# Kernel optimization log

Hardware: AMD Instinct MI355X
Metric: run time of the kernel (lower is better)

## Reference

```python
import jax, jax.numpy as jnp
import numpy as np

B, BAG, H, C = 512, 32, 1024, 53
EPS = 1e-8  # torch F.cosine_similarity denominator clamp


def setup_inputs() -> dict:
    key = jax.random.key(0)
    ks = jax.random.split(key, 5)
    return {
        "sent_reps": jax.random.normal(ks[0], (B, BAG, H), jnp.float32),
        "aug_sent_reps": jax.random.normal(ks[1], (B, BAG, H), jnp.float32),
        "rel_table": jax.random.normal(ks[2], (C, H), jnp.float32),
        "cls_w": jax.random.normal(ks[3], (C, H), jnp.float32) * 0.02,
        "cls_b": jnp.zeros((C,), jnp.float32),
        "labels": jax.random.randint(ks[4], (B,), 0, C),
        "temperature": jnp.asarray(0.1, jnp.float32),
    }


def _cl(rep, aug, bag_rep, T):
    # rep, aug: (B, bag, H); bag_rep: (B, H)
    nr = jnp.linalg.norm(rep, axis=-1)        # (B, bag)
    na = jnp.linalg.norm(aug, axis=-1)        # (B, bag)
    nb = jnp.linalg.norm(bag_rep, axis=-1)    # (B,)
    pos_sim = jnp.sum(rep * aug, axis=-1) / jnp.maximum(nr * na, EPS)  # (B, bag)
    pos = jnp.exp(pos_sim / T)
    # pair[c, j, b] = cos(rep[b, j], bag_rep[c])  -- matches torch permute/broadcast chain
    dots = jnp.einsum('bjh,ch->cjb', rep, bag_rep)               # (B, bag, B)
    denom = jnp.maximum(nb[:, None, None] * nr.T[None], EPS)      # (B, bag, B)
    pair = dots / denom
    idx = jnp.arange(rep.shape[0])
    axis_sim = pair[idx, :, idx]                                  # (B, bag): cos(rep[b,j], bag_rep[b])
    neg = jnp.exp(pair / T).sum(axis=2) - jnp.exp(axis_sim / T)   # (B, bag)
    return jnp.mean(-jnp.log(pos / (pos + neg)))


def reference(sent_reps, aug_sent_reps, rel_table, cls_w, cls_b, labels, temperature):
    # Selective attention per bag (scope slices are uniform bags of size BAG -> vectorized)
    rel = rel_table[labels]                                        # (B, H)
    scale = jnp.sqrt(jnp.asarray(H, sent_reps.dtype))
    scores = jnp.einsum('bh,bjh->bj', rel, sent_reps) / scale      # (B, bag)
    alphas = jax.nn.softmax(scores, axis=-1)
    bag_reps = jnp.einsum('bj,bjh->bh', alphas, sent_reps)         # (B, H)
    bag_out = bag_reps @ cls_w.T + cls_b                           # (B, C)  (dropout in eval = identity)
    cl_loss = _cl(sent_reps, aug_sent_reps, bag_reps, temperature)
    return bag_out, cl_loss
```

## Files before the change

### kernel.cpp

```cpp
#include <hip/hip_runtime.h>
#include <hip/hip_bf16.h>


typedef __bf16 bf16x8 __attribute__((ext_vector_type(8)));
typedef __bf16 bf16x4 __attribute__((ext_vector_type(4)));
typedef float  f32x4  __attribute__((ext_vector_type(4)));

__device__ inline float wsum(float v) {
    #pragma unroll
    for (int off = 32; off > 0; off >>= 1) v += __shfl_xor(v, off, 64);
    return v;
}

__device__ inline void gll16(const void* g, void* l) {
    __builtin_amdgcn_global_load_lds((const __attribute__((address_space(1))) void*)g,
                                     (__attribute__((address_space(3))) void*)l, 16, 0, 0);
}

__global__ __launch_bounds__(256) void k0_cvt(const float* __restrict__ w, __bf16* __restrict__ wb,
                                              float* __restrict__ nbsq)
{
    int i = blockIdx.x * 256 + threadIdx.x;
    wb[i] = (i < 53 * 1024) ? (__bf16)w[i] : (__bf16)0.0f;
    if (i < 512) nbsq[i] = 0.0f;
}

__global__ __launch_bounds__(256) void k12(
    const float* __restrict__ sent, const float* __restrict__ aug,
    const float* __restrict__ rel_table, const int* __restrict__ labels,
    __bf16* __restrict__ bagb, float* __restrict__ nbsq,
    __bf16* __restrict__ repb, float* __restrict__ nr, float* __restrict__ pos_sim,
    float* __restrict__ scoreg, float* __restrict__ alphag)
{
    __shared__ __bf16 Vb[32 * 1024];
    const int b = blockIdx.x, t = threadIdx.x;
    const int j = t >> 3, seg = t & 7;
    const int lane = t & 63;

    const size_t rbase = (size_t)(b * 32 + j) * 1024;
    const float* srow = sent + rbase;
    const float* arow = aug + rbase;
    const float* relp = rel_table + (size_t)labels[b] * 1024;

    float P = 0.f, R = 0.f, A = 0.f, D = 0.f;
    #pragma unroll 8
    for (int i = 0; i < 32; i++) {
        const int h = i * 32 + seg * 4;
        f32x4 v  = *(const f32x4*)(srow + h);
        f32x4 a  = *(const f32x4*)(arow + h);
        f32x4 rl = *(const f32x4*)(relp + h);
        P += v.x * rl.x + v.y * rl.y + v.z * rl.z + v.w * rl.w;
        R += v.x * v.x + v.y * v.y + v.z * v.z + v.w * v.w;
        A += a.x * a.x + a.y * a.y + a.z * a.z + a.w * a.w;
        D += v.x * a.x + v.y * a.y + v.z * a.z + v.w * a.w;
        bf16x4 vb = { (__bf16)v.x, (__bf16)v.y, (__bf16)v.z, (__bf16)v.w };
        *(bf16x4*)(&Vb[j * 1024 + (i ^ (j & 1)) * 32 + seg * 4]) = vb;
        *(bf16x4*)(repb + rbase + h) = vb;
    }
    #pragma unroll
    for (int off = 1; off <= 4; off <<= 1) {
        P += __shfl_xor(P, off, 64);
        R += __shfl_xor(R, off, 64);
        A += __shfl_xor(A, off, 64);
        D += __shfl_xor(D, off, 64);
    }
    if (seg == 0) {
        scoreg[b * 32 + j] = P * (1.0f / 32.0f);
        float nrv = sqrtf(R), nav = sqrtf(A);
        nr[b * 32 + j] = nrv;
        pos_sim[b * 32 + j] = D / fmaxf(nrv * nav, 1e-8f);
    }
    __threadfence_block();
    __syncthreads();

    if (t < 32) {
        float sj = scoreg[b * 32 + t];
        float m = sj;
        #pragma unroll
        for (int off = 16; off > 0; off >>= 1) m = fmaxf(m, __shfl_xor(m, off, 32));
        float e = __expf(sj - m);
        float sum = e;
        #pragma unroll
        for (int off = 16; off > 0; off >>= 1) sum += __shfl_xor(sum, off, 32);
        alphag[b * 32 + t] = e / sum;
    }
    __threadfence_block();
    __syncthreads();

    f32x4 bag = {0.f, 0.f, 0.f, 0.f};
    #pragma unroll 8
    for (int jj = 0; jj < 32; jj++) {
        const float al = alphag[b * 32 + jj];
        bf16x4 vb = *(const bf16x4*)(&Vb[jj * 1024 + ((t >> 3) ^ (jj & 1)) * 32 + (t & 7) * 4]);
        bag.x += al * (float)vb.x;
        bag.y += al * (float)vb.y;
        bag.z += al * (float)vb.z;
        bag.w += al * (float)vb.w;
    }
    bf16x4 bb = { (__bf16)bag.x, (__bf16)bag.y, (__bf16)bag.z, (__bf16)bag.w };
    *(bf16x4*)(bagb + (size_t)b * 1024 + t * 4) = bb;

    float q = bag.x * bag.x + bag.y * bag.y + bag.z * bag.z + bag.w * bag.w;
    q = wsum(q);
    if (lane == 0) atomicAdd(&nbsq[b], q);
}

__global__ __launch_bounds__(256) void k3m(
    const __bf16* __restrict__ bagb, const __bf16* __restrict__ cwb,
    const float* __restrict__ bias, float* __restrict__ out)
{
    __shared__ __align__(16) __bf16 Al[64 * 32];
    __shared__ __align__(16) __bf16 Bl[64 * 32];
    const int r0 = blockIdx.x * 64;
    const int t = threadIdx.x, lane = t & 63, w = t >> 6;
    const int m = lane & 15, quad = lane >> 4;
    f32x4 acc[4] = {};

    const int i0 = t * 8;
    const int row0 = i0 >> 5, kk0 = i0 & 31;
    const __bf16* gA = bagb + (size_t)(r0 + row0) * 1024 + kk0;
    const __bf16* gB = cwb + (size_t)row0 * 1024 + kk0;

    for (int k0 = 0; k0 < 1024; k0 += 32) {
        __syncthreads();
        gll16(gA + k0, Al + i0);
        gll16(gB + k0, Bl + i0);
        __syncthreads();
        bf16x8 a = *(const bf16x8*)(&Al[(w * 16 + m) * 32 + quad * 8]);
        #pragma unroll
        for (int n = 0; n < 4; n++) {
            bf16x8 bf = *(const bf16x8*)(&Bl[(n * 16 + m) * 32 + quad * 8]);
            acc[n] = __builtin_amdgcn_mfma_f32_16x16x32_bf16(a, bf, acc[n], 0, 0, 0);
        }
    }
    #pragma unroll
    for (int n = 0; n < 4; n++) {
        const int c = n * 16 + m;
        if (c < 53) {
            #pragma unroll
            for (int i = 0; i < 4; i++) {
                const int r = r0 + w * 16 + quad * 4 + i;
                out[(size_t)r * 53 + c] = acc[n][i] + bias[c];
            }
        }
    }
}

__global__ __launch_bounds__(256) void k4_gemm(
    const __bf16* __restrict__ repb, const __bf16* __restrict__ bagb,
    const float* __restrict__ nr, const float* __restrict__ nbsq,
    const float* __restrict__ temp, __bf16* __restrict__ E)
{
    __shared__ __align__(16) __bf16 Al[128 * 32];
    __shared__ __align__(16) __bf16 Bl[128 * 32];
    const int bid = blockIdx.x;
    const int xcd = bid & 7, slot = bid >> 3;
    const int cb = slot & 3, rb = (slot >> 2) * 8 + xcd;
    const int r0 = rb * 128, c0 = cb * 128;
    const int t = threadIdx.x, lane = t & 63, w = t >> 6;
    const int m = lane & 15, quad = lane >> 4;
    const int wr0 = (w & 1) * 64, wc0 = (w >> 1) * 64;

    f32x4 acc[4][4] = {};

    const int i0 = t * 8, i1 = 2048 + t * 8;
    const int row0 = i0 >> 5, kk0 = i0 & 31;
    const int row1 = i1 >> 5, kk1 = i1 & 31;
    const __bf16* gA0 = repb + (size_t)(r0 + row0) * 1024 + kk0;
    const __bf16* gA1 = repb + (size_t)(r0 + row1) * 1024 + kk1;
    const __bf16* gB0 = bagb + (size_t)(c0 + row0) * 1024 + kk0;
    const __bf16* gB1 = bagb + (size_t)(c0 + row1) * 1024 + kk1;

    for (int k0 = 0; k0 < 1024; k0 += 32) {
        __syncthreads();
        gll16(gA0 + k0, Al + i0);
        gll16(gA1 + k0, Al + i1);
        gll16(gB0 + k0, Bl + i0);
        gll16(gB1 + k0, Bl + i1);
        __syncthreads();
        bf16x8 a[4], bf[4];
        #pragma unroll
        for (int i = 0; i < 4; i++) a[i]  = *(const bf16x8*)(&Al[(wr0 + i * 16 + m) * 32 + quad * 8]);
        #pragma unroll
        for (int n = 0; n < 4; n++) bf[n] = *(const bf16x8*)(&Bl[(wc0 + n * 16 + m) * 32 + quad * 8]);
        #pragma unroll
        for (int i = 0; i < 4; i++)
            #pragma unroll
            for (int n = 0; n < 4; n++)
                acc[i][n] = __builtin_amdgcn_mfma_f32_16x16x32_bf16(a[i], bf[n], acc[i][n], 0, 0, 0);
    }

    const float invT = 1.0f / *temp;
    float nrv[16];
    #pragma unroll
    for (int i = 0; i < 4; i++)
        #pragma unroll
        for (int g = 0; g < 4; g++)
            nrv[i * 4 + g] = nr[r0 + wr0 + i * 16 + quad * 4 + g];
    #pragma unroll
    for (int n = 0; n < 4; n++) {
        const int c = c0 + wc0 + n * 16 + m;
        const float nbv = sqrtf(nbsq[c]);
        #pragma unroll
        for (int i = 0; i < 4; i++) {
            #pragma unroll
            for (int g = 0; g < 4; g++) {
                const int r = r0 + wr0 + i * 16 + quad * 4 + g;
                float pair = acc[i][n][g] / fmaxf(nbv * nrv[i * 4 + g], 1e-8f);
                E[(size_t)r * 512 + c] = (__bf16)__expf(pair * invT);
            }
        }
    }
}

__global__ __launch_bounds__(256) void k5_neg(
    const __bf16* __restrict__ E, const float* __restrict__ pos_sim,
    const float* __restrict__ temp, float* __restrict__ bsums)
{
    const int ct = blockIdx.x & 7, j = blockIdx.x >> 3;
    const int t = threadIdx.x, lane = t & 63, w = t >> 6;
    const int c8 = t & 7;
    const int bsub = t >> 3;
    const size_t cbase = (size_t)ct * 64 + c8 * 8;

    float acc[8] = {};
    #pragma unroll 4
    for (int it = 0; it < 16; it++) {
        const int b = it * 32 + bsub;
        bf16x8 v = *(const bf16x8*)(E + (size_t)(b * 32 + j) * 512 + cbase);
        #pragma unroll
        for (int k = 0; k < 8; k++) acc[k] += (float)v[k];
    }
    #pragma unroll
    for (int k = 0; k < 8; k++) {
        acc[k] += __shfl_xor(acc[k], 8, 64);
        acc[k] += __shfl_xor(acc[k], 16, 64);
        acc[k] += __shfl_xor(acc[k], 32, 64);
    }
    __shared__ float red[4][64];
    if (lane < 8) {
        #pragma unroll
        for (int k = 0; k < 8; k++) red[w][lane * 8 + k] = acc[k];
    }
    __syncthreads();

    if (t < 64) {
        const int cc = ct * 64 + t;
        float S = red[0][t] + red[1][t] + red[2][t] + red[3][t];
        S -= (float)E[(size_t)((cc << 5) + j) * 512 + cc];
        const float invT = 1.0f / *temp;
        const float lp = pos_sim[(cc << 5) + j] * invT;
        float term = logf(__expf(lp) + S) - lp;
        term = wsum(term);
        if (t == 0) bsums[blockIdx.x] = term;
    }
}

__global__ __launch_bounds__(256) void k6_final(const float* __restrict__ bsums, float* __restrict__ loss)
{
    const int t = threadIdx.x;
    float v = bsums[t];
    v = wsum(v);
    __shared__ float r[4];
    if ((t & 63) == 0) r[t >> 6] = v;
    __syncthreads();
    if (t == 0) *loss = (r[0] + r[1] + r[2] + r[3]) * (1.0f / 16384.0f);
}

extern "C" void kernel_launch(void* const* d_in, const int* in_sizes, int n_in,
                              void* d_out, int out_size, void* d_ws, size_t ws_size,
                              hipStream_t stream)
{
    const float* sent = (const float*)d_in[0];
    const float* aug  = (const float*)d_in[1];
    const float* rel  = (const float*)d_in[2];
    const float* clsw = (const float*)d_in[3];
    const float* clsb = (const float*)d_in[4];
    const int*   lab  = (const int*)d_in[5];
    const float* temp = (const float*)d_in[6];
    float* out = (float*)d_out;

    char* ws = (char*)d_ws;
    __bf16* bagb   = (__bf16*)(ws);
    float*  nbsq   = (float*)(ws + (1u << 20));
    float*  nr     = (float*)(ws + (1u << 20) + 64 * 1024);
    float*  pos    = (float*)(ws + (1u << 20) + 128 * 1024);
    __bf16* cwb    = (__bf16*)(ws + (1u << 20) + 192 * 1024);
    float*  scoreg = (float*)(ws + (1u << 20) + 320 * 1024);
    float*  alphag = (float*)(ws + (1u << 20) + 384 * 1024);
    float*  bsums  = (float*)(ws + (2u << 20));
    __bf16* repb   = (__bf16*)(ws + (4u << 20));
    __bf16* E      = (__bf16*)(ws + (36u << 20));

    k0_cvt  <<<256, 256, 0, stream>>>(clsw, cwb, nbsq);
    k12     <<<512, 256, 0, stream>>>(sent, aug, rel, lab, bagb, nbsq, repb, nr, pos, scoreg, alphag);
    k3m     <<<8, 256, 0, stream>>>(bagb, cwb, clsb, out);
    k4_gemm <<<512, 256, 0, stream>>>(repb, bagb, nr, nbsq, temp, E);
    k5_neg  <<<256, 256, 0, stream>>>(E, pos, temp, bsums);
    k6_final<<<1, 256, 0, stream>>>(bsums, out + 27136);
}
```

Baseline: 220.4 us.

## Fuse exp-sum partial reduction into GEMM epilogue, widen k12 blocks to 512 threads

The similarity GEMM epilogue no longer writes the full bf16 exp matrix (16M entries). It sums over the 4 row-blocks of each bag inside LDS, writes fp32 partial sums per (row-block, j, column), and records diagonal terms separately, so k5 reads a much smaller partial buffer. k12 moves to 512 threads with a new LDS swizzle, and scores and alphas are kept in shared memory instead of global. k3m now processes K in steps of 64. The trade-off is extra LDS and a barrier in the GEMM epilogue, and the diagonal logic is fiddly.

```diff
diff --git a/kernel.cpp b/kernel.cpp
--- a/kernel.cpp
+++ b/kernel.cpp
@@ -4,6 +4,7 @@
 
 typedef __bf16 bf16x8 __attribute__((ext_vector_type(8)));
 typedef __bf16 bf16x4 __attribute__((ext_vector_type(4)));
+typedef __bf16 bf16x2 __attribute__((ext_vector_type(2)));
 typedef float  f32x4  __attribute__((ext_vector_type(4)));
 
 __device__ inline float wsum(float v) {
@@ -25,16 +26,17 @@
     if (i < 512) nbsq[i] = 0.0f;
 }
 
-__global__ __launch_bounds__(256) void k12(
+__global__ __launch_bounds__(512, 4) void k12(
     const float* __restrict__ sent, const float* __restrict__ aug,
     const float* __restrict__ rel_table, const int* __restrict__ labels,
     __bf16* __restrict__ bagb, float* __restrict__ nbsq,
-    __bf16* __restrict__ repb, float* __restrict__ nr, float* __restrict__ pos_sim,
-    float* __restrict__ scoreg, float* __restrict__ alphag)
+    __bf16* __restrict__ repb, float* __restrict__ nr, float* __restrict__ pos_sim)
 {
     __shared__ __bf16 Vb[32 * 1024];
+    __shared__ float scoreS[32];
+    __shared__ float alphaS[32];
     const int b = blockIdx.x, t = threadIdx.x;
-    const int j = t >> 3, seg = t & 7;
+    const int j = t >> 4, seg = t & 15;
     const int lane = t & 63;
 
     const size_t rbase = (size_t)(b * 32 + j) * 1024;
@@ -43,9 +45,9 @@
     const float* relp = rel_table + (size_t)labels[b] * 1024;
 
     float P = 0.f, R = 0.f, A = 0.f, D = 0.f;
-    #pragma unroll 8
-    for (int i = 0; i < 32; i++) {
-        const int h = i * 32 + seg * 4;
+    #pragma unroll 4
+    for (int i = 0; i < 16; i++) {
+        const int h = i * 64 + seg * 4;
         f32x4 v  = *(const f32x4*)(srow + h);
         f32x4 a  = *(const f32x4*)(arow + h);
         f32x4 rl = *(const f32x4*)(relp + h);
@@ -54,27 +56,27 @@
         A += a.x * a.x + a.y * a.y + a.z * a.z + a.w * a.w;
         D += v.x * a.x + v.y * a.y + v.z * a.z + v.w * a.w;
         bf16x4 vb = { (__bf16)v.x, (__bf16)v.y, (__bf16)v.z, (__bf16)v.w };
-        *(bf16x4*)(&Vb[j * 1024 + (i ^ (j & 1)) * 32 + seg * 4]) = vb;
+        const int g = i * 16 + seg;
+        *(bf16x4*)(&Vb[j * 1024 + (g ^ (j & 15)) * 4]) = vb;
         *(bf16x4*)(repb + rbase + h) = vb;
     }
     #pragma unroll
-    for (int off = 1; off <= 4; off <<= 1) {
+    for (int off = 1; off <= 8; off <<= 1) {
         P += __shfl_xor(P, off, 64);
         R += __shfl_xor(R, off, 64);
         A += __shfl_xor(A, off, 64);
         D += __shfl_xor(D, off, 64);
     }
     if (seg == 0) {
-        scoreg[b * 32 + j] = P * (1.0f / 32.0f);
+        scoreS[j] = P * (1.0f / 32.0f);
         float nrv = sqrtf(R), nav = sqrtf(A);
         nr[b * 32 + j] = nrv;
         pos_sim[b * 32 + j] = D / fmaxf(nrv * nav, 1e-8f);
     }
-    __threadfence_block();
     __syncthreads();
 
     if (t < 32) {
-        float sj = scoreg[b * 32 + t];
+        float sj = scoreS[t];
         float m = sj;
         #pragma unroll
         for (int off = 16; off > 0; off >>= 1) m = fmaxf(m, __shfl_xor(m, off, 32));
@@ -82,25 +84,23 @@
         float sum = e;
         #pragma unroll
         for (int off = 16; off > 0; off >>= 1) sum += __shfl_xor(sum, off, 32);
-        alphag[b * 32 + t] = e / sum;
-    }
-    __threadfence_block();
-    __syncthreads();
-
-    f32x4 bag = {0.f, 0.f, 0.f, 0.f};
+        alphaS[t] = e / sum;
+    }
+    __syncthreads();
+
+    float ax = 0.f, ay = 0.f;
+    const int g2 = t >> 1, sub = t & 1;
     #pragma unroll 8
     for (int jj = 0; jj < 32; jj++) {
-        const float al = alphag[b * 32 + jj];
-        bf16x4 vb = *(const bf16x4*)(&Vb[jj * 1024 + ((t >> 3) ^ (jj & 1)) * 32 + (t & 7) * 4]);
-        bag.x += al * (float)vb.x;
-        bag.y += al * (float)vb.y;
-        bag.z += al * (float)vb.z;
-        bag.w += al * (float)vb.w;
-    }
-    bf16x4 bb = { (__bf16)bag.x, (__bf16)bag.y, (__bf16)bag.z, (__bf16)bag.w };
-    *(bf16x4*)(bagb + (size_t)b * 1024 + t * 4) = bb;
-
-    float q = bag.x * bag.x + bag.y * bag.y + bag.z * bag.z + bag.w * bag.w;
+        const float al = alphaS[jj];
+        bf16x2 v2 = *(const bf16x2*)(&Vb[jj * 1024 + (g2 ^ (jj & 15)) * 4 + sub * 2]);
+        ax += al * (float)v2.x;
+        ay += al * (float)v2.y;
+    }
+    bf16x2 bb = { (__bf16)ax, (__bf16)ay };
+    *(bf16x2*)(bagb + (size_t)b * 1024 + t * 2) = bb;
+
+    float q = ax * ax + ay * ay;
     q = wsum(q);
     if (lane == 0) atomicAdd(&nbsq[b], q);
 }
@@ -109,8 +109,8 @@
     const __bf16* __restrict__ bagb, const __bf16* __restrict__ cwb,
     const float* __restrict__ bias, float* __restrict__ out)
 {
-    __shared__ __align__(16) __bf16 Al[64 * 32];
-    __shared__ __align__(16) __bf16 Bl[64 * 32];
+    __shared__ __align__(16) __bf16 Al[2 * 2048];
+    __shared__ __align__(16) __bf16 Bl[2 * 2048];
     const int r0 = blockIdx.x * 64;
     const int t = threadIdx.x, lane = t & 63, w = t >> 6;
     const int m = lane & 15, quad = lane >> 4;
@@ -121,16 +121,21 @@
     const __bf16* gA = bagb + (size_t)(r0 + row0) * 1024 + kk0;
     const __bf16* gB = cwb + (size_t)row0 * 1024 + kk0;
 
-    for (int k0 = 0; k0 < 1024; k0 += 32) {
+    for (int k0 = 0; k0 < 1024; k0 += 64) {
         __syncthreads();
-        gll16(gA + k0, Al + i0);
-        gll16(gB + k0, Bl + i0);
+        gll16(gA + k0,      Al + i0);
+        gll16(gA + k0 + 32, Al + 2048 + i0);
+        gll16(gB + k0,      Bl + i0);
+        gll16(gB + k0 + 32, Bl + 2048 + i0);
         __syncthreads();
-        bf16x8 a = *(const bf16x8*)(&Al[(w * 16 + m) * 32 + quad * 8]);
-        #pragma unroll
-        for (int n = 0; n < 4; n++) {
-            bf16x8 bf = *(const bf16x8*)(&Bl[(n * 16 + m) * 32 + quad * 8]);
-            acc[n] = __builtin_amdgcn_mfma_f32_16x16x32_bf16(a, bf, acc[n], 0, 0, 0);
+        #pragma unroll
+        for (int ks = 0; ks < 2; ks++) {
+            bf16x8 a = *(const bf16x8*)(&Al[ks * 2048 + (w * 16 + m) * 32 + quad * 8]);
+            #pragma unroll
+            for (int n = 0; n < 4; n++) {
+                bf16x8 bf = *(const bf16x8*)(&Bl[ks * 2048 + (n * 16 + m) * 32 + quad * 8]);
+                acc[n] = __builtin_amdgcn_mfma_f32_16x16x32_bf16(a, bf, acc[n], 0, 0, 0);
+            }
         }
     }
     #pragma unroll
@@ -149,10 +154,11 @@
 __global__ __launch_bounds__(256) void k4_gemm(
     const __bf16* __restrict__ repb, const __bf16* __restrict__ bagb,
     const float* __restrict__ nr, const float* __restrict__ nbsq,
-    const float* __restrict__ temp, __bf16* __restrict__ E)
+    const float* __restrict__ temp, float* __restrict__ partial, float* __restrict__ diag)
 {
     __shared__ __align__(16) __bf16 Al[128 * 32];
     __shared__ __align__(16) __bf16 Bl[128 * 32];
+    __shared__ float negp[2][32][128];
     const int bid = blockIdx.x;
     const int xcd = bid & 7, slot = bid >> 3;
     const int cb = slot & 3, rb = (slot >> 2) * 8 + xcd;
@@ -160,6 +166,10 @@
     const int t = threadIdx.x, lane = t & 63, w = t >> 6;
     const int m = lane & 15, quad = lane >> 4;
     const int wr0 = (w & 1) * 64, wc0 = (w >> 1) * 64;
+    const int half = w & 1;
+
+    #pragma unroll
+    for (int z = 0; z < 32; z++) ((float*)negp)[z * 256 + t] = 0.f;
 
     f32x4 acc[4][4] = {};
 
@@ -197,59 +207,75 @@
         #pragma unroll
         for (int g = 0; g < 4; g++)
             nrv[i * 4 + g] = nr[r0 + wr0 + i * 16 + quad * 4 + g];
+
     #pragma unroll
     for (int n = 0; n < 4; n++) {
-        const int c = c0 + wc0 + n * 16 + m;
-        const float nbv = sqrtf(nbsq[c]);
-        #pragma unroll
-        for (int i = 0; i < 4; i++) {
+        const int c_local = wc0 + n * 16 + m;
+        const int cg = c0 + c_local;
+        const float nbv = sqrtf(nbsq[cg]);
+        #pragma unroll
+        for (int i = 0; i < 2; i++) {
             #pragma unroll
             for (int g = 0; g < 4; g++) {
-                const int r = r0 + wr0 + i * 16 + quad * 4 + g;
-                float pair = acc[i][n][g] / fmaxf(nbv * nrv[i * 4 + g], 1e-8f);
-                E[(size_t)r * 512 + c] = (__bf16)__expf(pair * invT);
+                const int jj = i * 16 + quad * 4 + g;
+                const int rg0 = r0 + wr0 + i * 16 + quad * 4 + g;
+                const int rg2 = rg0 + 32;
+                float e0 = __expf(acc[i][n][g]     / fmaxf(nbv * nrv[i * 4 + g],       1e-8f) * invT);
+                float e2 = __expf(acc[i + 2][n][g] / fmaxf(nbv * nrv[(i + 2) * 4 + g], 1e-8f) * invT);
+                negp[half][jj][c_local] = e0 + e2;
+                if ((rg0 >> 5) == cg) diag[(size_t)cg * 32 + jj] = e0;
+                if ((rg2 >> 5) == cg) diag[(size_t)cg * 32 + jj] = e2;
             }
         }
     }
+    __syncthreads();
+
+    float* pout = partial + (size_t)rb * 32 * 512 + c0;
+    #pragma unroll
+    for (int v = 0; v < 4; v++) {
+        const int idx = v * 1024 + t * 4;
+        const int jj = idx >> 7, cl = idx & 127;
+        f32x4 a = *(const f32x4*)(&negp[0][jj][cl]);
+        f32x4 bq = *(const f32x4*)(&negp[1][jj][cl]);
+        f32x4 s = a + bq;
+        *(f32x4*)(pout + (size_t)jj * 512 + cl) = s;
+    }
 }
 
 __global__ __launch_bounds__(256) void k5_neg(
-    const __bf16* __restrict__ E, const float* __restrict__ pos_sim,
-    const float* __restrict__ temp, float* __restrict__ bsums)
+    const float* __restrict__ partial, const float* __restrict__ diag,
+    const float* __restrict__ pos_sim, const float* __restrict__ temp,
+    float* __restrict__ bsums)
 {
     const int ct = blockIdx.x & 7, j = blockIdx.x >> 3;
     const int t = threadIdx.x, lane = t & 63, w = t >> 6;
-    const int c8 = t & 7;
-    const int bsub = t >> 3;
-    const size_t cbase = (size_t)ct * 64 + c8 * 8;
-
-    float acc[8] = {};
+    const int bsub = t >> 4;
+    const int cidx = t & 15;
+    f32x4 acc = {};
     #pragma unroll 4
-    for (int it = 0; it < 16; it++) {
-        const int b = it * 32 + bsub;
-        bf16x8 v = *(const bf16x8*)(E + (size_t)(b * 32 + j) * 512 + cbase);
-        #pragma unroll
-        for (int k = 0; k < 8; k++) acc[k] += (float)v[k];
-    }
-    #pragma unroll
-    for (int k = 0; k < 8; k++) {
-        acc[k] += __shfl_xor(acc[k], 8, 64);
+    for (int r = 0; r < 8; r++) {
+        const int rb = bsub * 8 + r;
+        f32x4 v = *(const f32x4*)(partial + ((size_t)rb * 32 + j) * 512 + ct * 64 + cidx * 4);
+        acc += v;
+    }
+    #pragma unroll
+    for (int k = 0; k < 4; k++) {
         acc[k] += __shfl_xor(acc[k], 16, 64);
         acc[k] += __shfl_xor(acc[k], 32, 64);
     }
     __shared__ float red[4][64];
-    if (lane < 8) {
-        #pragma unroll
-        for (int k = 0; k < 8; k++) red[w][lane * 8 + k] = acc[k];
+    if (lane < 16) {
+        #pragma unroll
+        for (int k = 0; k < 4; k++) red[w][lane * 4 + k] = acc[k];
     }
     __syncthreads();
 
     if (t < 64) {
-        const int cc = ct * 64 + t;
+        const int c = ct * 64 + t;
         float S = red[0][t] + red[1][t] + red[2][t] + red[3][t];
-        S -= (float)E[(size_t)((cc << 5) + j) * 512 + cc];
+        S -= diag[(size_t)c * 32 + j];
         const float invT = 1.0f / *temp;
-        const float lp = pos_sim[(cc << 5) + j] * invT;
+        const float lp = pos_sim[(c << 5) + j] * invT;
         float term = logf(__expf(lp) + S) - lp;
         term = wsum(term);
         if (t == 0) bsums[blockIdx.x] = term;
@@ -281,21 +307,20 @@
     float* out = (float*)d_out;
 
     char* ws = (char*)d_ws;
-    __bf16* bagb   = (__bf16*)(ws);
-    float*  nbsq   = (float*)(ws + (1u << 20));
-    float*  nr     = (float*)(ws + (1u << 20) + 64 * 1024);
-    float*  pos    = (float*)(ws + (1u << 20) + 128 * 1024);
-    __bf16* cwb    = (__bf16*)(ws + (1u << 20) + 192 * 1024);
-    float*  scoreg = (float*)(ws + (1u << 20) + 320 * 1024);
-    float*  alphag = (float*)(ws + (1u << 20) + 384 * 1024);
-    float*  bsums  = (float*)(ws + (2u << 20));
-    __bf16* repb   = (__bf16*)(ws + (4u << 20));
-    __bf16* E      = (__bf16*)(ws + (36u << 20));
+    __bf16* bagb    = (__bf16*)(ws);
+    float*  nbsq    = (float*)(ws + (1u << 20));
+    float*  nr      = (float*)(ws + (1u << 20) + 64 * 1024);
+    float*  pos     = (float*)(ws + (1u << 20) + 128 * 1024);
+    __bf16* cwb     = (__bf16*)(ws + (1u << 20) + 192 * 1024);
+    float*  bsums   = (float*)(ws + (2u << 20));
+    float*  diag    = (float*)(ws + (2u << 20) + 64 * 1024);
+    __bf16* repb    = (__bf16*)(ws + (4u << 20));
+    float*  partial = (float*)(ws + (36u << 20));
 
     k0_cvt  <<<256, 256, 0, stream>>>(clsw, cwb, nbsq);
-    k12     <<<512, 256, 0, stream>>>(sent, aug, rel, lab, bagb, nbsq, repb, nr, pos, scoreg, alphag);
+    k12     <<<512, 512, 0, stream>>>(sent, aug, rel, lab, bagb, nbsq, repb, nr, pos);
     k3m     <<<8, 256, 0, stream>>>(bagb, cwb, clsb, out);
-    k4_gemm <<<512, 256, 0, stream>>>(repb, bagb, nr, nbsq, temp, E);
-    k5_neg  <<<256, 256, 0, stream>>>(E, pos, temp, bsums);
+    k4_gemm <<<512, 256, 0, stream>>>(repb, bagb, nr, nbsq, temp, partial, diag);
+    k5_neg  <<<256, 256, 0, stream>>>(partial, diag, pos, temp, bsums);
     k6_final<<<1, 256, 0, stream>>>(bsums, out + 27136);
 }
```

New measurement: 215.3 us. 2.3% less time.
